# Optimization experiments

Measured on AMD Instinct MI355X. Metric: run time of the kernel, lower is better.

## Reference

```python
import jax, jax.numpy as jnp
import numpy as np

N_NODES = 50000
N_EDGES = 800000
DIM = 128
N_LAYERS = 3
OUT_DIM = 2
W_SCALE = 0.02


def setup_inputs() -> dict:
    key = jax.random.key(0)
    ks = jax.random.split(key, 12)
    x = jax.random.normal(ks[0], (N_NODES, DIM), dtype=jnp.float32)
    src = jax.random.randint(ks[1], (N_EDGES,), 0, N_NODES, dtype=jnp.int32)
    dst = jax.random.randint(ks[2], (N_EDGES,), 0, N_NODES, dtype=jnp.int32)
    Vw = jax.random.normal(ks[3], (N_LAYERS, DIM, DIM), dtype=jnp.float32) * W_SCALE
    Vb = jax.random.normal(ks[4], (N_LAYERS, DIM), dtype=jnp.float32) * W_SCALE
    Aw = jax.random.normal(ks[5], (N_LAYERS, DIM, DIM), dtype=jnp.float32) * W_SCALE
    Ab = jax.random.normal(ks[6], (N_LAYERS, DIM), dtype=jnp.float32) * W_SCALE
    Rw = jax.random.normal(ks[7], (N_LAYERS, DIM, DIM), dtype=jnp.float32) * W_SCALE
    Rb = jax.random.normal(ks[8], (N_LAYERS, DIM), dtype=jnp.float32) * W_SCALE
    out_w = jax.random.normal(ks[9], (OUT_DIM, DIM), dtype=jnp.float32) * W_SCALE
    out_b = jax.random.normal(ks[10], (OUT_DIM,), dtype=jnp.float32) * W_SCALE
    return {"x": x, "src": src, "dst": dst, "Vw": Vw, "Vb": Vb, "Aw": Aw,
            "Ab": Ab, "Rw": Rw, "Rb": Rb, "out_w": out_w, "out_b": out_b}


def reference(x, src, dst, Vw, Vb, Aw, Ab, Rw, Rb, out_w, out_b):
    # x: [N, d]; src/dst: [E] (edge (dst_i <- src_i): out[dst] += h[src], as torch.spmm(Adj, h))
    N = x.shape[0]
    h = x
    for l in range(Vw.shape[0]):
        # sum aggregation over neighbors; learn_eps=False adds self-loops -> + h
        agg = jax.ops.segment_sum(h[src], dst, num_segments=N) + h  # [N, d]
        ro = jnp.sum(h, axis=0, keepdims=True)                      # sum readout, [1, d]
        # trainable combine: relu(V(h) + A(agg) + R(readout)), R term broadcasts over nodes
        h = jax.nn.relu(h @ Vw[l].T + Vb[l]
                        + agg @ Aw[l].T + Ab[l]
                        + ro @ Rw[l].T + Rb[l])
    # node task, recursive_weighting=False: sigmoid(Linear(h))
    return jax.nn.sigmoid(h @ out_w.T + out_b)
```

## Files before the change

kernel.cpp:

```cpp
#include <hip/hip_runtime.h>
#include <cstdint>
#include <cstddef>

#define NN 50000
#define NE 800000
#define D 128
#define KK 256
#define NPAD 50048
#define LDSW 136
#define BSTR 136
#define NBUCK 196
#define BCAP 5120
#define ECH 8192
#define EBLKS ((NE + ECH - 1) / ECH)
#define CVT_BLOCKS 391
#define AGG_BLOCKS 12500

typedef __bf16 bf16x8 __attribute__((ext_vector_type(8)));
typedef float f32x4 __attribute__((ext_vector_type(4)));
typedef float f32x2 __attribute__((ext_vector_type(2)));
typedef unsigned short ushort;
typedef unsigned int uint;

__device__ __forceinline__ ushort f2b(float f) {
    uint u = __float_as_uint(f);
    uint r = (u + 0x7fffu + ((u >> 16) & 1u)) >> 16;
    return (ushort)r;
}
__device__ __forceinline__ float blo(uint u) { return __uint_as_float(u << 16); }
__device__ __forceinline__ float bhi(uint u) { return __uint_as_float(u & 0xffff0000u); }

__device__ __forceinline__ uint enc_n(float v) {
    int t = (int)(__float_as_uint(v) >> 22);
    int n = max(t - 252, min(t - 251, 1));
    return (uint)min(max(n, 0), 7);
}
__device__ __forceinline__ uint enc8(uint4 vv, float sf) {
    uint n0 = enc_n(blo(vv.x) * sf), n1 = enc_n(bhi(vv.x) * sf);
    uint n2 = enc_n(blo(vv.y) * sf), n3 = enc_n(bhi(vv.y) * sf);
    uint n4 = enc_n(blo(vv.z) * sf), n5 = enc_n(bhi(vv.z) * sf);
    uint n6 = enc_n(blo(vv.w) * sf), n7 = enc_n(bhi(vv.w) * sf);
    return n0 | (n1 << 4) | (n2 << 8) | (n3 << 12) |
           (n4 << 16) | (n5 << 20) | (n6 << 24) | (n7 << 28);
}
__device__ __forceinline__ void dec_acc(uint u, float* a) {
    uint lo = u & 0x0F0F0F0Fu;
    uint hi = (u >> 4) & 0x0F0F0F0Fu;
    uint b0 = __builtin_amdgcn_perm(0x4C484440u, 0x3C383000u, lo);
    uint b1 = __builtin_amdgcn_perm(0x4C484440u, 0x3C383000u, hi);
    f32x2 p;
    p = __builtin_amdgcn_cvt_pk_f32_fp8(b0, false); a[0] += p.x; a[2] += p.y;
    p = __builtin_amdgcn_cvt_pk_f32_fp8(b0, true);  a[4] += p.x; a[6] += p.y;
    p = __builtin_amdgcn_cvt_pk_f32_fp8(b1, false); a[1] += p.x; a[3] += p.y;
    p = __builtin_amdgcn_cvt_pk_f32_fp8(b1, true);  a[5] += p.x; a[7] += p.y;
}

__global__ void k_prep(int* __restrict__ zone, const float* __restrict__ Vw,
                       const float* __restrict__ Aw, ushort* __restrict__ W2) {
    int b = blockIdx.x, t = threadIdx.x;
    if (b < 4) {
        zone[b * 256 + t] = 0;
        return;
    }
    int idx = (b - 4) * 256 + t;
    int k = idx & (KK - 1);
    int j = (idx >> 8) & (D - 1);
    int l = idx >> 15;
    float v = (k < D) ? Vw[((size_t)l * D + j) * D + k]
                      : Aw[((size_t)l * D + j) * D + (k - D)];
    W2[idx] = f2b(v);
}

__global__ void __launch_bounds__(256) k_scatcvt(
    const int* __restrict__ src, const int* __restrict__ dst,
    int* __restrict__ bfill, uint* __restrict__ packed,
    const float* __restrict__ x, ushort* __restrict__ hb,
    uint* __restrict__ hf4, float* __restrict__ ro0) {
    int t = threadIdx.x;
    if (blockIdx.x < EBLKS) {
        __shared__ int cnt[NBUCK];
        __shared__ int base[NBUCK];
        if (t < NBUCK) cnt[t] = 0;
        __syncthreads();
        int e0 = blockIdx.x * ECH, e1 = min(e0 + ECH, NE);
        for (int e = e0 + t; e < e1; e += 256) atomicAdd(&cnt[dst[e] >> 8], 1);
        __syncthreads();
        if (t < NBUCK) base[t] = cnt[t] ? (atomicAdd(&bfill[t], cnt[t]) + t * BCAP) : 0;
        __syncthreads();
        for (int e = e0 + t; e < e1; e += 256) {
            int d = dst[e];
            int b = d >> 8;
            int p = atomicAdd(&base[b], 1);
            packed[p] = (uint)src[e] | ((uint)(d & 255) << 16);
        }
        return;
    }
    __shared__ float scol[D];
    if (t < D) scol[t] = 0.f;
    __syncthreads();
    const float4* x4 = (const float4*)x;
    uint4* h8 = (uint4*)hb;
    float cs[8] = {0, 0, 0, 0, 0, 0, 0, 0};
    int base = (blockIdx.x - EBLKS) * 2048 + t;
#pragma unroll
    for (int i = 0; i < 8; i++) {
        int idx = base + i * 256;
        if (idx < NN * D / 8) {
            float4 va = x4[idx * 2], vb = x4[idx * 2 + 1];
            cs[0] += va.x; cs[1] += va.y; cs[2] += va.z; cs[3] += va.w;
            cs[4] += vb.x; cs[5] += vb.y; cs[6] += vb.z; cs[7] += vb.w;
            uint4 o;
            o.x = (uint)f2b(va.x) | ((uint)f2b(va.y) << 16);
            o.y = (uint)f2b(va.z) | ((uint)f2b(va.w) << 16);
            o.z = (uint)f2b(vb.x) | ((uint)f2b(vb.y) << 16);
            o.w = (uint)f2b(vb.z) | ((uint)f2b(vb.w) << 16);
            h8[idx] = o;
            uint n0 = enc_n(fmaxf(va.x * 0.75f + 3.f, 0.f));
            uint n1 = enc_n(fmaxf(va.y * 0.75f + 3.f, 0.f));
            uint n2 = enc_n(fmaxf(va.z * 0.75f + 3.f, 0.f));
            uint n3 = enc_n(fmaxf(va.w * 0.75f + 3.f, 0.f));
            uint n4 = enc_n(fmaxf(vb.x * 0.75f + 3.f, 0.f));
            uint n5 = enc_n(fmaxf(vb.y * 0.75f + 3.f, 0.f));
            uint n6 = enc_n(fmaxf(vb.z * 0.75f + 3.f, 0.f));
            uint n7 = enc_n(fmaxf(vb.w * 0.75f + 3.f, 0.f));
            hf4[idx] = n0 | (n1 << 4) | (n2 << 8) | (n3 << 12) |
                       (n4 << 16) | (n5 << 20) | (n6 << 24) | (n7 << 28);
        }
    }
#pragma unroll
    for (int k = 0; k < 8; k++) {
        cs[k] += __shfl_xor(cs[k], 16);
        cs[k] += __shfl_xor(cs[k], 32);
    }
    if ((t & 63) < 16) {
        int c8 = (t & 15) * 8;
#pragma unroll
        for (int k = 0; k < 8; k++) atomicAdd(&scol[c8 + k], cs[k]);
    }
    __syncthreads();
    if (t < D) atomicAdd(&ro0[t], scol[t]);
}

__global__ void k_bcsr(const uint* __restrict__ packed, const int* __restrict__ bfill,
                       int* __restrict__ esrc, int2* __restrict__ rp2) {
    __shared__ int hist[256];
    __shared__ int sc[256];
    __shared__ int fill[256];
    int b = blockIdx.x, t = threadIdx.x;
    int lo = b * BCAP, cnt = bfill[b];
    hist[t] = 0;
    __syncthreads();
    for (int i = t; i < cnt; i += 256) atomicAdd(&hist[packed[lo + i] >> 16], 1);
    __syncthreads();
    int v = hist[t];
    sc[t] = v;
    __syncthreads();
    for (int off = 1; off < 256; off <<= 1) {
        int u = (t >= off) ? sc[t - off] : 0;
        __syncthreads();
        sc[t] += u;
        __syncthreads();
    }
    int excl = sc[t] - v;
    int node = b * 256 + t;
    if (node < NN) rp2[node] = make_int2(lo + excl, lo + excl + v);
    fill[t] = lo + excl;
    __syncthreads();
    for (int i = t; i < cnt; i += 256) {
        uint p = packed[lo + i];
        int pos = atomicAdd(&fill[p >> 16], 1);
        esrc[pos] = (int)(p & 0xffffu);
    }
}


__global__ void k_agg(const ushort* __restrict__ hb, const uint* __restrict__ hf4,
                      const int2* __restrict__ rp2, const int* __restrict__ esrc,
                      const float* __restrict__ slot, ushort* __restrict__ A1,
                      int lay0, const float* __restrict__ ro,
                      const float* __restrict__ Rw, const float* __restrict__ Vb,
                      const float* __restrict__ Ab, const float* __restrict__ Rb,
                      float* __restrict__ rbias, float* __restrict__ slot_next) {
    if (blockIdx.x >= AGG_BLOCKS) {
        int j = blockIdx.x - AGG_BLOCKS;
        int l = threadIdx.x;
        if (l < 64) {
            float s = ro[l] * Rw[(size_t)j * D + l] +
                      ro[l + 64] * Rw[(size_t)j * D + l + 64];
#pragma unroll
            for (int off = 32; off; off >>= 1) s += __shfl_xor(s, off);
            if (l == 0) {
                float r = Vb[j] + Ab[j] + Rb[j] + s;
                rbias[j] = r;
                atomicMax((int*)slot_next, __float_as_int(fabsf(r)));
            }
        }
        return;
    }
    int wave = (blockIdx.x * blockDim.x + threadIdx.x) >> 6;
    int lane = threadIdx.x & 63;
    if (wave >= NN) return;
    int c = lane & 15, s = lane >> 4;
    float dsc = lay0 ? (4.f / 3.f) : fmaxf(slot[0], 0.5f) * (1.f / 3.f);
    float doff = lay0 ? 4.f : 0.f;
    float a[8] = {0, 0, 0, 0, 0, 0, 0, 0};
    int2 rp = rp2[wave];
    int e0 = rp.x, e1 = rp.y;
    int cnt = e1 - e0;
    int iters = (cnt + 3) >> 2;
    int i0 = e0 + s;
    for (int it = 0; it < iters; it += 4) {
        int ia = i0 + it * 4, ib = ia + 4, ic = ia + 8, id = ia + 12;
        uint ua = 0, ub = 0, uc = 0, ud = 0;
        if (ia < e1) ua = hf4[esrc[ia] * 16 + c];
        if (ib < e1) ub = hf4[esrc[ib] * 16 + c];
        if (ic < e1) uc = hf4[esrc[ic] * 16 + c];
        if (id < e1) ud = hf4[esrc[id] * 16 + c];
        dec_acc(ua, a);
        dec_acc(ub, a);
        dec_acc(uc, a);
        dec_acc(ud, a);
    }
#pragma unroll
    for (int k = 0; k < 8; k++) {
        a[k] += __shfl_xor(a[k], 16);
        a[k] += __shfl_xor(a[k], 32);
    }
    if (s == 0) {
        float cf = (float)cnt * doff;
        uint4 su = ((const uint4*)(hb + (size_t)wave * D))[c];
        float r0 = a[0] * dsc - cf + blo(su.x);
        float r1 = a[1] * dsc - cf + bhi(su.x);
        float r2 = a[2] * dsc - cf + blo(su.y);
        float r3 = a[3] * dsc - cf + bhi(su.y);
        float r4 = a[4] * dsc - cf + blo(su.z);
        float r5 = a[5] * dsc - cf + bhi(su.z);
        float r6 = a[6] * dsc - cf + blo(su.w);
        float r7 = a[7] * dsc - cf + bhi(su.w);
        uint4 o;
        o.x = (uint)f2b(r0) | ((uint)f2b(r1) << 16);
        o.y = (uint)f2b(r2) | ((uint)f2b(r3) << 16);
        o.z = (uint)f2b(r4) | ((uint)f2b(r5) << 16);
        o.w = (uint)f2b(r6) | ((uint)f2b(r7) << 16);
        ((uint4*)(A1 + (size_t)wave * D))[c] = o;
    }
}

template <bool LAST>
__global__ void __launch_bounds__(256) k_gemm(const ushort* __restrict__ hbin,
                                              const ushort* __restrict__ A1,
                                              const ushort* __restrict__ W2,
                                              const float* __restrict__ rbias,
                                              const float* __restrict__ sclw,
                                              ushort* __restrict__ hout,
                                              uint* __restrict__ hf4,
                                              float* __restrict__ ro_next,
                                              const float* __restrict__ ow,
                                              const float* __restrict__ ob,
                                              float* __restrict__ outp) {
    __shared__ ushort lds[D * BSTR];
    __shared__ float scol[D];
    int t = threadIdx.x;
    if (!LAST) {
        if (t < D) scol[t] = 0.f;
    }
    {
        const uint4* ws = (const uint4*)W2;
#pragma unroll
        for (int i = 0; i < 16; i++) {
            int idx = t + i * 256;
            int row = idx >> 5;
            int cu = idx & 31;
            *(uint4*)(lds + row * BSTR + cu * 8) = ws[idx];
        }
    }
    __syncthreads();

    int wave = t >> 6, lane = t & 63;
    int m = lane & 15, q = lane >> 4;
    int node0 = blockIdx.x * 64 + wave * 16;

    f32x4 acc[8];
#pragma unroll
    for (int j = 0; j < 8; j++) acc[j] = (f32x4){0.f, 0.f, 0.f, 0.f};

    const ushort* aself = hbin + (size_t)(node0 + m) * D + q * 8;
    const ushort* aagg  = A1   + (size_t)(node0 + m) * D + q * 8;
    const ushort* bl = lds + m * BSTR + q * 8;
#pragma unroll
    for (int kt = 0; kt < 8; kt++) {
        int k0 = (kt & 3) * 32;
        const ushort* ab = (kt < 4) ? aself : aagg;
        bf16x8 a = *(const bf16x8*)(ab + k0);
#pragma unroll
        for (int j = 0; j < 8; j++) {
            bf16x8 b = *(const bf16x8*)(bl + j * 16 * BSTR + kt * 32);
            acc[j] = __builtin_amdgcn_mfma_f32_16x16x32_bf16(a, b, acc[j], 0, 0, 0);
        }
    }
    __syncthreads();

    float rb[8];
#pragma unroll
    for (int j = 0; j < 8; j++) rb[j] = rbias[j * 16 + m];
    ushort* mytile = lds + wave * 16 * LDSW;
    float psum[8] = {0, 0, 0, 0, 0, 0, 0, 0};
#pragma unroll
    for (int j = 0; j < 8; j++) {
        f32x4 v = acc[j];
#pragma unroll
        for (int r = 0; r < 4; r++) {
            int row = q * 4 + r;
            float val = fmaxf(v[r] + rb[j], 0.f);
            if (!LAST) { if (node0 + row < NN) psum[j] += val; }
            mytile[row * LDSW + j * 16 + m] = f2b(val);
        }
    }

    if (!LAST) {
#pragma unroll
        for (int j = 0; j < 8; j++) atomicAdd(&scol[j * 16 + m], psum[j]);
        float sf = 3.f / fmaxf(sclw[0], 0.5f);
#pragma unroll
        for (int it = 0; it < 4; it++) {
            int row = it * 4 + q;
            int grow = node0 + row;
            if (grow < NN) {
                uint4 vv = *(const uint4*)(mytile + row * LDSW + m * 8);
                *(uint4*)(hout + (size_t)grow * D + m * 8) = vv;
                hf4[(size_t)grow * 16 + m] = enc8(vv, sf);
            }
        }
        __syncthreads();
        if (t < D) atomicAdd(&ro_next[t], scol[t]);
    } else {
        float2 a0 = ((const float2*)ow)[lane];
        float2 a1 = ((const float2*)(ow + D))[lane];
        float b0 = ob[0], b1 = ob[1];
        for (int r = 0; r < 16; r++) {
            int node = node0 + r;
            uint u = ((const uint*)(mytile + r * LDSW))[lane];
            float vx = blo(u), vy = bhi(u);
            float p0 = vx * a0.x + vy * a0.y;
            float p1 = vx * a1.x + vy * a1.y;
#pragma unroll
            for (int off = 32; off; off >>= 1) {
                p0 += __shfl_xor(p0, off);
                p1 += __shfl_xor(p1, off);
            }
            if (lane == 0 && node < NN) {
                outp[(size_t)node * 2 + 0] = 1.f / (1.f + expf(-(p0 + b0)));
                outp[(size_t)node * 2 + 1] = 1.f / (1.f + expf(-(p1 + b1)));
            }
        }
    }
}

extern "C" void kernel_launch(void* const* d_in, const int* in_sizes, int n_in,
                              void* d_out, int out_size, void* d_ws, size_t ws_size,
                              hipStream_t stream) {
    const float* x   = (const float*)d_in[0];
    const int*   src = (const int*)d_in[1];
    const int*   dst = (const int*)d_in[2];
    const float* Vw  = (const float*)d_in[3];
    const float* Vb  = (const float*)d_in[4];
    const float* Aw  = (const float*)d_in[5];
    const float* Ab  = (const float*)d_in[6];
    const float* Rw  = (const float*)d_in[7];
    const float* Rb  = (const float*)d_in[8];
    const float* ow  = (const float*)d_in[9];
    const float* ob  = (const float*)d_in[10];
    float* out = (float*)d_out;

    char* w = (char*)d_ws;
    ushort* hb0    = (ushort*)w; w += (size_t)NPAD * D * 2;
    ushort* hb1    = (ushort*)w; w += (size_t)NPAD * D * 2;
    ushort* A1     = (ushort*)w; w += (size_t)NPAD * D * 2;
    uint*   hf4    = (uint*)w;   w += (size_t)NN * 16 * 4;
    ushort* W2     = (ushort*)w; w += (size_t)3 * D * KK * 2;
    int*    zone   = (int*)w;    w += (size_t)1024 * 4;
    float*  ro     = (float*)zone;
    float*  scl    = (float*)(zone + 512);
    int*    bfill  = zone + 520;
    uint*   packed = (uint*)w;   w += (size_t)NBUCK * BCAP * 4;
    int*    esrc   = (int*)w;    w += (size_t)NBUCK * BCAP * 4;
    int2*   rp2    = (int2*)w;   w += (size_t)NN * 8;
    float*  rbias  = (float*)w;  w += (size_t)D * 4;

    k_prep<<<4 + 384, 256, 0, stream>>>(zone, Vw, Aw, W2);
    k_scatcvt<<<EBLKS + CVT_BLOCKS, 256, 0, stream>>>(src, dst, bfill, packed,
                                                      x, hb0, hf4, ro);
    k_bcsr<<<NBUCK, 256, 0, stream>>>(packed, bfill, esrc, rp2);

    const ushort* hin = hb0;
    ushort* hbufs[2] = {hb1, hb0};
    for (int l = 0; l < 3; l++) {
        k_agg<<<AGG_BLOCKS + D, 256, 0, stream>>>(
            hin, hf4, rp2, esrc, scl + l, A1, l == 0 ? 1 : 0,
            ro + (size_t)l * D, Rw + (size_t)l * D * D, Vb + (size_t)l * D,
            Ab + (size_t)l * D, Rb + (size_t)l * D, rbias, scl + l + 1);
        ushort* hnext = hbufs[l & 1];
        if (l < 2) {
            k_gemm<false><<<NPAD / 64, 256, 0, stream>>>(
                hin, A1, W2 + (size_t)l * D * KK, rbias, scl + l + 1, hnext, hf4,
                ro + (size_t)(l + 1) * D, nullptr, nullptr, nullptr);
        } else {
            k_gemm<true><<<NPAD / 64, 256, 0, stream>>>(
                hin, A1, W2 + (size_t)l * D * KK, rbias, nullptr, nullptr, nullptr,
                nullptr, ow, ob, out);
        }
        hin = hnext;
    }
}
```

Baseline: 302.7 us.

## Split scatter and convert kernels, record per-edge slot to avoid second atomic pass

Splits the combined scatter/convert kernel into two separate launches and halves the edge chunk size so more scatter blocks run. Both the bucket scatter and the CSR build now store each element's intra-bucket offset in LDS during the counting pass, so the placement pass no longer needs a second round of LDS atomics. This trades an extra kernel launch and more LDS per block for fewer contended atomics. It also makes the placement order within a node deterministic per block.

After: 299.1 us. Within noise of the previous version (-1.2%).

```diff
diff --git a/kernel.cpp b/kernel.cpp
--- a/kernel.cpp
+++ b/kernel.cpp
@@ -11,8 +11,8 @@
 #define BSTR 136
 #define NBUCK 196
 #define BCAP 5120
-#define ECH 8192
-#define EBLKS ((NE + ECH - 1) / ECH)
+#define SCH 4096
+#define SBLKS ((NE + SCH - 1) / SCH)
 #define CVT_BLOCKS 391
 #define AGG_BLOCKS 12500
 
@@ -71,37 +71,42 @@
     W2[idx] = f2b(v);
 }
 
-__global__ void __launch_bounds__(256) k_scatcvt(
+__global__ void __launch_bounds__(256) k_scat(
     const int* __restrict__ src, const int* __restrict__ dst,
-    int* __restrict__ bfill, uint* __restrict__ packed,
+    int* __restrict__ bfill, uint* __restrict__ packed) {
+    __shared__ int cnt[256];
+    __shared__ int base[256];
+    __shared__ ushort pos[SCH];
+    int t = threadIdx.x;
+    int e0 = blockIdx.x * SCH, e1 = min(e0 + SCH, NE);
+    cnt[t] = 0;
+    __syncthreads();
+    for (int e = e0 + t; e < e1; e += 256) {
+        int b = dst[e] >> 8;
+        pos[e - e0] = (ushort)atomicAdd(&cnt[b], 1);
+    }
+    __syncthreads();
+    if (t < NBUCK && cnt[t])
+        base[t] = atomicAdd(&bfill[t], cnt[t]) + t * BCAP;
+    __syncthreads();
+    for (int e = e0 + t; e < e1; e += 256) {
+        int d = dst[e];
+        int b = d >> 8;
+        packed[base[b] + pos[e - e0]] = (uint)src[e] | ((uint)(d & 255) << 16);
+    }
+}
+
+__global__ void __launch_bounds__(256) k_cvt(
     const float* __restrict__ x, ushort* __restrict__ hb,
     uint* __restrict__ hf4, float* __restrict__ ro0) {
+    __shared__ float scol[D];
     int t = threadIdx.x;
-    if (blockIdx.x < EBLKS) {
-        __shared__ int cnt[NBUCK];
-        __shared__ int base[NBUCK];
-        if (t < NBUCK) cnt[t] = 0;
-        __syncthreads();
-        int e0 = blockIdx.x * ECH, e1 = min(e0 + ECH, NE);
-        for (int e = e0 + t; e < e1; e += 256) atomicAdd(&cnt[dst[e] >> 8], 1);
-        __syncthreads();
-        if (t < NBUCK) base[t] = cnt[t] ? (atomicAdd(&bfill[t], cnt[t]) + t * BCAP) : 0;
-        __syncthreads();
-        for (int e = e0 + t; e < e1; e += 256) {
-            int d = dst[e];
-            int b = d >> 8;
-            int p = atomicAdd(&base[b], 1);
-            packed[p] = (uint)src[e] | ((uint)(d & 255) << 16);
-        }
-        return;
-    }
-    __shared__ float scol[D];
     if (t < D) scol[t] = 0.f;
     __syncthreads();
     const float4* x4 = (const float4*)x;
     uint4* h8 = (uint4*)hb;
     float cs[8] = {0, 0, 0, 0, 0, 0, 0, 0};
-    int base = (blockIdx.x - EBLKS) * 2048 + t;
+    int base = blockIdx.x * 2048 + t;
 #pragma unroll
     for (int i = 0; i < 8; i++) {
         int idx = base + i * 256;
@@ -145,12 +150,16 @@
                        int* __restrict__ esrc, int2* __restrict__ rp2) {
     __shared__ int hist[256];
     __shared__ int sc[256];
-    __shared__ int fill[256];
+    __shared__ int start[256];
+    __shared__ ushort pos[BCAP];
     int b = blockIdx.x, t = threadIdx.x;
     int lo = b * BCAP, cnt = bfill[b];
     hist[t] = 0;
     __syncthreads();
-    for (int i = t; i < cnt; i += 256) atomicAdd(&hist[packed[lo + i] >> 16], 1);
+    for (int i = t; i < cnt; i += 256) {
+        int node = (packed[lo + i] >> 16) & 255;
+        pos[i] = (ushort)atomicAdd(&hist[node], 1);
+    }
     __syncthreads();
     int v = hist[t];
     sc[t] = v;
@@ -164,12 +173,11 @@
     int excl = sc[t] - v;
     int node = b * 256 + t;
     if (node < NN) rp2[node] = make_int2(lo + excl, lo + excl + v);
-    fill[t] = lo + excl;
+    start[t] = lo + excl;
     __syncthreads();
     for (int i = t; i < cnt; i += 256) {
         uint p = packed[lo + i];
-        int pos = atomicAdd(&fill[p >> 16], 1);
-        esrc[pos] = (int)(p & 0xffffu);
+        esrc[start[(p >> 16) & 255] + pos[i]] = (int)(p & 0xffffu);
     }
 }
 
@@ -388,8 +396,8 @@
     float*  rbias  = (float*)w;  w += (size_t)D * 4;
 
     k_prep<<<4 + 384, 256, 0, stream>>>(zone, Vw, Aw, W2);
-    k_scatcvt<<<EBLKS + CVT_BLOCKS, 256, 0, stream>>>(src, dst, bfill, packed,
-                                                      x, hb0, hf4, ro);
+    k_scat<<<SBLKS, 256, 0, stream>>>(src, dst, bfill, packed);
+    k_cvt<<<CVT_BLOCKS, 256, 0, stream>>>(x, hb0, hf4, ro);
     k_bcsr<<<NBUCK, 256, 0, stream>>>(packed, bfill, esrc, rp2);
 
     const ushort* hin = hb0;
```
